# Kernel tuning notes

Hardware: AMD Instinct MI355X
Metric: run time of the kernel (lower is better)

Reference implementation:

```python
import jax, jax.numpy as jnp
import numpy as np

N_NODES = 50000
N_EDGES = 600000
D = 128
N_GRAPHS = 64


def setup_inputs() -> dict:
    key = jax.random.key(0)
    ks = jax.random.split(key, 16)
    x = jax.random.normal(ks[0], (N_NODES, D), dtype=jnp.float32)
    edge_index = jax.random.randint(ks[1], (2, N_EDGES), 0, N_NODES, dtype=jnp.int64)
    batch = jnp.sort(jax.random.randint(ks[2], (N_NODES,), 0, N_GRAPHS, dtype=jnp.int64))
    s = 1.0 / np.sqrt(D)
    def lin(k, out_d, in_d):
        return jax.random.uniform(k, (out_d, in_d), jnp.float32, -s, s)
    inp = {"x": x, "edge_index": edge_index, "batch": batch}
    for i, base in zip(range(3), (3, 6, 9)):
        inp[f"W_rel{i+1}"] = lin(ks[base], D, D)
        inp[f"b_rel{i+1}"] = jax.random.uniform(ks[base + 1], (D,), jnp.float32, -s, s)
        inp[f"W_root{i+1}"] = lin(ks[base + 2], D, D)
    s5 = 1.0 / np.sqrt(5)
    inp["W1"] = lin(ks[12], 5, D)
    inp["b1"] = jax.random.uniform(ks[13], (5,), jnp.float32, -s, s)
    inp["W2"] = jax.random.uniform(ks[14], (1, 5), jnp.float32, -s5, s5)
    inp["b2"] = jax.random.uniform(ks[15], (1,), jnp.float32, -s5, s5)
    return inp


def graph_conv(x, src, dst, W_rel, b_rel, W_root):
    # PyG GraphConv: out_i = W_root x_i + W_rel * sum_{j->i} x_j + b_rel
    agg = jax.ops.segment_sum(x[src], dst, num_segments=N_NODES)  # [N, D]
    return agg @ W_rel.T + b_rel + x @ W_root.T


def reference(x, edge_index, batch,
              W_rel1, b_rel1, W_root1,
              W_rel2, b_rel2, W_root2,
              W_rel3, b_rel3, W_root3,
              W1, b1, W2, b2):
    src, dst = edge_index[0], edge_index[1]
    h = jax.nn.relu(graph_conv(x, src, dst, W_rel1, b_rel1, W_root1))
    h = jax.nn.relu(graph_conv(h, src, dst, W_rel2, b_rel2, W_root2))
    h = graph_conv(h, src, dst, W_rel3, b_rel3, W_root3)
    # global max pool over graphs
    g = jax.ops.segment_max(h, batch, num_segments=N_GRAPHS)  # [G, D]
    out = jax.nn.relu(g @ W1.T + b1) @ W2.T + b2  # [G, 1]
    return out
```

## Files before the change

kernel.cpp:

```cpp
#include <hip/hip_runtime.h>
#include <float.h>

#define N_NODES 50000
#define N_EDGES 600000
#define D 128
#define N_GRAPHS 64
#define SCAN_T 256
#define SCAN_NBLK ((N_NODES + SCAN_T - 1) / SCAN_T)

typedef __attribute__((ext_vector_type(8))) short short8;
typedef __attribute__((ext_vector_type(4))) float floatx4;

__device__ inline float bf2f(unsigned short h) {
    return __uint_as_float((unsigned)h << 16);
}
__device__ inline unsigned short f2bf(float f) {
    unsigned u = __float_as_uint(f);
    return (unsigned short)((u + 0x7fffu + ((u >> 16) & 1u)) >> 16);
}

#define ACCQ(u, ss) {                                                            \
    int w0_ = (u).x, w1_ = (u).y, w2_ = (u).z, w3_ = (u).w;                      \
    a[ 0] += (float)(signed char)(w0_      ) * (ss);                             \
    a[ 1] += (float)(signed char)(w0_ >>  8) * (ss);                             \
    a[ 2] += (float)(signed char)(w0_ >> 16) * (ss);                             \
    a[ 3] += (float)(w0_ >> 24)              * (ss);                             \
    a[ 4] += (float)(signed char)(w1_      ) * (ss);                             \
    a[ 5] += (float)(signed char)(w1_ >>  8) * (ss);                             \
    a[ 6] += (float)(signed char)(w1_ >> 16) * (ss);                             \
    a[ 7] += (float)(w1_ >> 24)              * (ss);                             \
    a[ 8] += (float)(signed char)(w2_      ) * (ss);                             \
    a[ 9] += (float)(signed char)(w2_ >>  8) * (ss);                             \
    a[10] += (float)(signed char)(w2_ >> 16) * (ss);                             \
    a[11] += (float)(w2_ >> 24)              * (ss);                             \
    a[12] += (float)(signed char)(w3_      ) * (ss);                             \
    a[13] += (float)(signed char)(w3_ >>  8) * (ss);                             \
    a[14] += (float)(signed char)(w3_ >> 16) * (ss);                             \
    a[15] += (float)(w3_ >> 24)              * (ss); }


__global__ __launch_bounds__(256) void cast_prep(
    const float* __restrict__ x,
    unsigned short* __restrict__ xb, signed char* __restrict__ xq,
    float* __restrict__ xs,
    const float* __restrict__ Wr0, const float* __restrict__ Wo0,
    const float* __restrict__ Wr1, const float* __restrict__ Wo1,
    const float* __restrict__ Wr2, const float* __restrict__ Wo2,
    unsigned short* __restrict__ B0, unsigned short* __restrict__ B1,
    unsigned short* __restrict__ B2,
    int* __restrict__ deg, float* __restrict__ g)
{
    int t = blockIdx.x * 256 + threadIdx.x;
    if (t < N_NODES * 16) {
        int node = t >> 4, ln = t & 15;
        const float4* xr = (const float4*)(x + (size_t)node * D + ln * 8);
        float4 v0 = xr[0], v1 = xr[1];
        float v[8] = {v0.x, v0.y, v0.z, v0.w, v1.x, v1.y, v1.z, v1.w};
        float am = 0.f;
#pragma unroll
        for (int i = 0; i < 8; ++i) am = fmaxf(am, fabsf(v[i]));
#pragma unroll
        for (int m = 1; m < 16; m <<= 1) am = fmaxf(am, __shfl_xor(am, m, 16));
        float inv = (am > 0.f) ? 127.f / am : 0.f;
        short8 hb;
#pragma unroll
        for (int i = 0; i < 8; ++i) hb[i] = (short)f2bf(v[i]);
        *(short8*)(xb + (size_t)node * D + ln * 8) = hb;
        int q0 = 0, q1 = 0;
#pragma unroll
        for (int i = 0; i < 4; ++i) { int q = (int)rintf(v[i]     * inv); q0 |= (q & 0xff) << (8 * i); }
#pragma unroll
        for (int i = 0; i < 4; ++i) { int q = (int)rintf(v[4 + i] * inv); q1 |= (q & 0xff) << (8 * i); }
        int2 qp; qp.x = q0; qp.y = q1;
        *(int2*)(xq + (size_t)node * D + ln * 8) = qp;
        if (ln == 0) xs[node] = am * (1.f / 127.f);
        return;
    }
    int w = t - N_NODES * 16;
    if (w < 3 * 128 * 256) {
        int l = w >> 15;
        int r = w & 32767;
        int o = r >> 8, k = r & 255;
        const float* Wr = (l == 0) ? Wr0 : (l == 1) ? Wr1 : Wr2;
        const float* Wo = (l == 0) ? Wo0 : (l == 1) ? Wo1 : Wo2;
        unsigned short* B = (l == 0) ? B0 : (l == 1) ? B1 : B2;
        float v = (k < 128) ? Wr[o * 128 + k] : Wo[o * 128 + (k - 128)];
        B[r] = f2bf(v);
        return;
    }
    w -= 3 * 128 * 256;
    if (w < N_NODES) { deg[w] = 0; return; }
    w -= N_NODES;
    if (w < N_GRAPHS * D) g[w] = -FLT_MAX;
}


__global__ void count_deg(const int* __restrict__ ei, int* __restrict__ deg) {
    int e = blockIdx.x * 256 + threadIdx.x;
    if (e < N_EDGES) atomicAdd(&deg[ei[N_EDGES + e]], 1);
}

__global__ __launch_bounds__(SCAN_T) void block_sum(const int* __restrict__ deg,
                                                    int* __restrict__ blockSums) {
    __shared__ int s[SCAN_T];
    int tid = threadIdx.x;
    int i = blockIdx.x * SCAN_T + tid;
    s[tid] = (i < N_NODES) ? deg[i] : 0;
    __syncthreads();
    for (int off = SCAN_T / 2; off > 0; off >>= 1) {
        if (tid < off) s[tid] += s[tid + off];
        __syncthreads();
    }
    if (tid == 0) blockSums[blockIdx.x] = s[0];
}

__global__ __launch_bounds__(SCAN_T) void scan_write(const int* __restrict__ deg,
                                                     const int* __restrict__ blockSums,
                                                     int* __restrict__ row_start,
                                                     int* __restrict__ cursor) {
    __shared__ int bs[SCAN_T];
    __shared__ int s[SCAN_T];
    int tid = threadIdx.x;
    bs[tid] = (tid < SCAN_NBLK) ? blockSums[tid] : 0;
    __syncthreads();
    for (int off = 1; off < SCAN_T; off <<= 1) {
        int tt = (tid >= off) ? bs[tid - off] : 0;
        __syncthreads();
        bs[tid] += tt;
        __syncthreads();
    }
    int myOff = (blockIdx.x == 0) ? 0 : bs[blockIdx.x - 1];
    if (blockIdx.x == 0 && tid == SCAN_T - 1) row_start[N_NODES] = bs[tid];

    int i = blockIdx.x * SCAN_T + tid;
    int v = (i < N_NODES) ? deg[i] : 0;
    s[tid] = v;
    __syncthreads();
    for (int off = 1; off < SCAN_T; off <<= 1) {
        int tt = (tid >= off) ? s[tid - off] : 0;
        __syncthreads();
        s[tid] += tt;
        __syncthreads();
    }
    if (i < N_NODES) {
        int rs = myOff + s[tid] - v;
        row_start[i] = rs;
        cursor[i]    = rs;
    }
}

__global__ void fill_csr(const int* __restrict__ ei, int* __restrict__ cursor,
                         int* __restrict__ csr_src) {
    int e = blockIdx.x * 256 + threadIdx.x;
    if (e < N_EDGES) {
        int dst = ei[N_EDGES + e];
        int pos = atomicAdd(&cursor[dst], 1);
        csr_src[pos] = ei[e];
    }
}


__global__ __launch_bounds__(256) void gather_q(
    const signed char* __restrict__ xq, const float* __restrict__ xs,
    const int* __restrict__ row_start, const int* __restrict__ csr_src,
    unsigned short* __restrict__ aggb)
{
    int grp  = threadIdx.x >> 3;
    int ln   = threadIdx.x & 7;
    int node = blockIdx.x * 32 + grp;
    if (node >= N_NODES) return;
    int beg = row_start[node];
    int end = row_start[node + 1];

    float a[16];
#pragma unroll
    for (int i = 0; i < 16; ++i) a[i] = 0.f;

    for (int base = beg; base < end; base += 8) {
        int n = end - base; if (n > 8) n = 8;
        int idx = (ln < n) ? csr_src[base + ln] : 0;
        int j = 0;
        for (; j + 3 < n; j += 4) {
            int s0 = __shfl(idx, j,     8); int s1 = __shfl(idx, j + 1, 8);
            int s2 = __shfl(idx, j + 2, 8); int s3 = __shfl(idx, j + 3, 8);
            int4 u0 = *(const int4*)(xq + (size_t)s0 * D + ln * 16);
            int4 u1 = *(const int4*)(xq + (size_t)s1 * D + ln * 16);
            int4 u2 = *(const int4*)(xq + (size_t)s2 * D + ln * 16);
            int4 u3 = *(const int4*)(xq + (size_t)s3 * D + ln * 16);
            float ss0 = xs[s0], ss1 = xs[s1], ss2 = xs[s2], ss3 = xs[s3];
            ACCQ(u0, ss0); ACCQ(u1, ss1); ACCQ(u2, ss2); ACCQ(u3, ss3);
        }
        for (; j < n; ++j) {
            int s0 = __shfl(idx, j, 8);
            int4 u0 = *(const int4*)(xq + (size_t)s0 * D + ln * 16);
            float ss0 = xs[s0];
            ACCQ(u0, ss0);
        }
    }
    short8 r0, r1;
#pragma unroll
    for (int i = 0; i < 8; ++i) { r0[i] = (short)f2bf(a[i]); r1[i] = (short)f2bf(a[8 + i]); }
    *(short8*)(aggb + (size_t)node * D + ln * 16)     = r0;
    *(short8*)(aggb + (size_t)node * D + ln * 16 + 8) = r1;
}


__device__ inline void stage_b_half(unsigned short* sB, const unsigned short* __restrict__ Bb,
                                    int tid, int h) {
#pragma unroll
    for (int i = 0; i < 8; ++i) {
        int flat = tid + i * 256;
        int fi = flat >> 6, ln = flat & 63;
        int mm = ln & 15, qq = ln >> 4;
        int ksL = fi >> 3, tt = fi & 7;
        short8 v = *(const short8*)(Bb + (size_t)(tt * 16 + mm) * 256
                                    + (h * 4 + ksL) * 32 + qq * 8);
        *(short8*)(sB + (size_t)flat * 8) = v;
    }
}


struct GemmShared {
    union {
        unsigned short b[16384];
        float c[64 * 130];
    };
};

__global__ __launch_bounds__(256) void gemm_mfma(
    const unsigned short* __restrict__ aggb, const unsigned short* __restrict__ xb,
    const unsigned short* __restrict__ Bb, const float* __restrict__ bias,
    unsigned short* __restrict__ Ob, signed char* __restrict__ Oq,
    float* __restrict__ Os)
{
    __shared__ GemmShared sh;
    int tid  = threadIdx.x;
    int wave = tid >> 6;
    int lane = tid & 63;
    int m    = lane & 15;
    int quad = lane >> 4;
    int row0 = blockIdx.x * 64 + wave * 16;

    int arow = row0 + m;
    if (arow > N_NODES - 1) arow = N_NODES - 1;

    short8 af[8];
#pragma unroll
    for (int ks = 0; ks < 8; ++ks) {
        const unsigned short* Asrc = (ks < 4) ? aggb : xb;
        af[ks] = *(const short8*)(Asrc + (size_t)arow * 128 + (ks & 3) * 32 + quad * 8);
    }

    floatx4 acc[8];
#pragma unroll
    for (int t = 0; t < 8; ++t) acc[t] = (floatx4){0.f, 0.f, 0.f, 0.f};

    stage_b_half(sh.b, Bb, tid, 0);
    __syncthreads();
#pragma unroll
    for (int ksL = 0; ksL < 4; ++ksL)
#pragma unroll
        for (int t = 0; t < 8; ++t) {
            short8 b = *(const short8*)(sh.b + (size_t)((ksL * 8 + t) * 64 + lane) * 8);
            acc[t] = __builtin_amdgcn_mfma_f32_16x16x32_bf16(af[ksL], b, acc[t], 0, 0, 0);
        }
    __syncthreads();
    stage_b_half(sh.b, Bb, tid, 1);
    __syncthreads();
#pragma unroll
    for (int ksL = 0; ksL < 4; ++ksL)
#pragma unroll
        for (int t = 0; t < 8; ++t) {
            short8 b = *(const short8*)(sh.b + (size_t)((ksL * 8 + t) * 64 + lane) * 8);
            acc[t] = __builtin_amdgcn_mfma_f32_16x16x32_bf16(af[4 + ksL], b, acc[t], 0, 0, 0);
        }
    __syncthreads();

#pragma unroll
    for (int t = 0; t < 8; ++t) {
        int col = t * 16 + m;
        float bv = bias[col];
#pragma unroll
        for (int r = 0; r < 4; ++r) {
            float v = fmaxf(acc[t][r] + bv, 0.f);
            sh.c[(wave * 16 + quad * 4 + r) * 130 + col] = v;
        }
    }
    __syncthreads();

    int lr  = tid >> 2;
    int seg = tid & 3;
    int grow = blockIdx.x * 64 + lr;
    const float* cp = &sh.c[lr * 130 + seg * 32];
    float vv[32];
    float am = 0.f;
#pragma unroll
    for (int i = 0; i < 32; ++i) { vv[i] = cp[i]; am = fmaxf(am, fabsf(vv[i])); }
    am = fmaxf(am, __shfl_xor(am, 1));
    am = fmaxf(am, __shfl_xor(am, 2));
    float inv = (am > 0.f) ? 127.f / am : 0.f;

    if (grow < N_NODES) {
#pragma unroll
        for (int c8 = 0; c8 < 4; ++c8) {
            short8 hb;
#pragma unroll
            for (int i = 0; i < 8; ++i) hb[i] = (short)f2bf(vv[c8 * 8 + i]);
            *(short8*)(Ob + (size_t)grow * 128 + seg * 32 + c8 * 8) = hb;
        }
        int qd[8];
#pragma unroll
        for (int d = 0; d < 8; ++d) {
            int q = 0;
#pragma unroll
            for (int i = 0; i < 4; ++i) {
                int qq = (int)rintf(vv[d * 4 + i] * inv);
                q |= (qq & 0xff) << (8 * i);
            }
            qd[d] = q;
        }
        int4 p0; p0.x = qd[0]; p0.y = qd[1]; p0.z = qd[2]; p0.w = qd[3];
        int4 p1; p1.x = qd[4]; p1.y = qd[5]; p1.z = qd[6]; p1.w = qd[7];
        *(int4*)(Oq + (size_t)grow * 128 + seg * 32)      = p0;
        *(int4*)(Oq + (size_t)grow * 128 + seg * 32 + 16) = p1;
        if (seg == 0) Os[grow] = am * (1.f / 127.f);
    }
}


struct PoolShared {
    union {
        unsigned short b[16384];
        float c[64 * 129];
    };
};

__global__ __launch_bounds__(256) void gemm_pool(
    const unsigned short* __restrict__ aggb, const unsigned short* __restrict__ xb,
    const unsigned short* __restrict__ Bb, const float* __restrict__ bias,
    const int* __restrict__ batch, float* __restrict__ g)
{
    __shared__ PoolShared sh;
    __shared__ int bl[64];
    int tid  = threadIdx.x;
    int wave = tid >> 6;
    int lane = tid & 63;
    int m    = lane & 15;
    int quad = lane >> 4;
    int row0 = blockIdx.x * 64;

    int arow = row0 + wave * 16 + m;
    if (arow > N_NODES - 1) arow = N_NODES - 1;

    short8 af[8];
#pragma unroll
    for (int ks = 0; ks < 8; ++ks) {
        const unsigned short* Asrc = (ks < 4) ? aggb : xb;
        af[ks] = *(const short8*)(Asrc + (size_t)arow * 128 + (ks & 3) * 32 + quad * 8);
    }

    floatx4 acc[8];
#pragma unroll
    for (int t = 0; t < 8; ++t) acc[t] = (floatx4){0.f, 0.f, 0.f, 0.f};

    if (tid < 64) {
        int grow = row0 + tid;
        bl[tid] = (grow < N_NODES) ? batch[grow] : -1;
    }
    stage_b_half(sh.b, Bb, tid, 0);
    __syncthreads();
#pragma unroll
    for (int ksL = 0; ksL < 4; ++ksL)
#pragma unroll
        for (int t = 0; t < 8; ++t) {
            short8 b = *(const short8*)(sh.b + (size_t)((ksL * 8 + t) * 64 + lane) * 8);
            acc[t] = __builtin_amdgcn_mfma_f32_16x16x32_bf16(af[ksL], b, acc[t], 0, 0, 0);
        }
    __syncthreads();
    stage_b_half(sh.b, Bb, tid, 1);
    __syncthreads();
#pragma unroll
    for (int ksL = 0; ksL < 4; ++ksL)
#pragma unroll
        for (int t = 0; t < 8; ++t) {
            short8 b = *(const short8*)(sh.b + (size_t)((ksL * 8 + t) * 64 + lane) * 8);
            acc[t] = __builtin_amdgcn_mfma_f32_16x16x32_bf16(af[4 + ksL], b, acc[t], 0, 0, 0);
        }
    __syncthreads();

#pragma unroll
    for (int t = 0; t < 8; ++t) {
        int col = t * 16 + m;
        float bv = bias[col];
#pragma unroll
        for (int r = 0; r < 4; ++r)
            sh.c[(wave * 16 + quad * 4 + r) * 129 + col] = acc[t][r] + bv;
    }
    __syncthreads();

    int nvalid = min(64, N_NODES - row0);
    int b0 = bl[0], b1 = bl[nvalid - 1];
    int col  = tid & 127;
    int rbeg = (tid >> 7) * 32;
    for (int gg = b0; gg <= b1; ++gg) {
        float cur = -FLT_MAX;
#pragma unroll
        for (int r = 0; r < 32; ++r) {
            int rr = rbeg + r;
            float v = (bl[rr] == gg) ? sh.c[rr * 129 + col] : -FLT_MAX;
            cur = fmaxf(cur, v);
        }
        if (cur > -FLT_MAX) {
            float* ad = &g[gg * D + col];
            if (cur >= 0.f) atomicMax((int*)ad, __float_as_int(cur));
            else            atomicMin((unsigned int*)ad, __float_as_uint(cur));
        }
    }
}


__global__ __launch_bounds__(64) void mlp_head(const float* __restrict__ g,
                         const float* __restrict__ W1, const float* __restrict__ b1,
                         const float* __restrict__ W2, const float* __restrict__ b2,
                         float* __restrict__ out) {
    int gi = blockIdx.x;
    int lane = threadIdx.x;
    float x0 = g[gi * D + lane];
    float x1 = g[gi * D + 64 + lane];
    float o = b2[0];
#pragma unroll
    for (int j = 0; j < 5; ++j) {
        float p = x0 * W1[j * D + lane] + x1 * W1[j * D + 64 + lane];
#pragma unroll
        for (int off = 32; off > 0; off >>= 1) p += __shfl_xor(p, off, 64);
        o += fmaxf(p + b1[j], 0.f) * W2[j];
    }
    if (lane == 0) out[gi] = o;
}

extern "C" void kernel_launch(void* const* d_in, const int* in_sizes, int n_in,
                              void* d_out, int out_size, void* d_ws, size_t ws_size,
                              hipStream_t stream) {
    const float* x     = (const float*)d_in[0];
    const int*   ei    = (const int*)d_in[1];
    const int*   batch = (const int*)d_in[2];
    const float* Wrel[3]  = {(const float*)d_in[3], (const float*)d_in[6], (const float*)d_in[9]};
    const float* brel[3]  = {(const float*)d_in[4], (const float*)d_in[7], (const float*)d_in[10]};
    const float* Wroot[3] = {(const float*)d_in[5], (const float*)d_in[8], (const float*)d_in[11]};
    const float* W1 = (const float*)d_in[12];
    const float* b1 = (const float*)d_in[13];
    const float* W2 = (const float*)d_in[14];
    const float* b2 = (const float*)d_in[15];
    float* out = (float*)d_out;

    char* ws = (char*)d_ws;
    const size_t nodeB16 = (size_t)N_NODES * D * sizeof(unsigned short);
    const size_t nodeB8  = (size_t)N_NODES * D;
    unsigned short* xb   = (unsigned short*)(ws);
    unsigned short* h1b  = (unsigned short*)(ws + 1 * nodeB16);
    unsigned short* h2b  = (unsigned short*)(ws + 2 * nodeB16);
    unsigned short* aggb = (unsigned short*)(ws + 3 * nodeB16);
    char* p = ws + 4 * nodeB16;
    signed char* xq  = (signed char*)p;  p += nodeB8;
    signed char* h1q = (signed char*)p;  p += nodeB8;
    signed char* h2q = (signed char*)p;  p += nodeB8;
    float* xs  = (float*)p;  p += N_NODES * sizeof(float);
    float* h1s = (float*)p;  p += N_NODES * sizeof(float);
    float* h2s = (float*)p;  p += N_NODES * sizeof(float);
    unsigned short* Bb0 = (unsigned short*)p;   p += 128 * 256 * sizeof(unsigned short);
    unsigned short* Bb1 = (unsigned short*)p;   p += 128 * 256 * sizeof(unsigned short);
    unsigned short* Bb2 = (unsigned short*)p;   p += 128 * 256 * sizeof(unsigned short);
    float* g        = (float*)p;                p += N_GRAPHS * D * sizeof(float);
    int*   deg      = (int*)p;                  p += N_NODES * sizeof(int);
    int*   row_start= (int*)p;                  p += (N_NODES + 1) * sizeof(int);
    int*   cursor   = (int*)p;                  p += N_NODES * sizeof(int);
    int*   csr_src  = (int*)p;                  p += N_EDGES * sizeof(int);
    int*   blockSums= (int*)p;                  p += SCAN_NBLK * sizeof(int);

    const int cast_total = N_NODES * 16 + 3 * 128 * 256 + N_NODES + N_GRAPHS * D;
    cast_prep<<<(cast_total + 255) / 256, 256, 0, stream>>>(
        x, xb, xq, xs,
        Wrel[0], Wroot[0], Wrel[1], Wroot[1], Wrel[2], Wroot[2],
        Bb0, Bb1, Bb2, deg, g);

    count_deg<<<(N_EDGES + 255) / 256, 256, 0, stream>>>(ei, deg);
    block_sum<<<SCAN_NBLK, SCAN_T, 0, stream>>>(deg, blockSums);
    scan_write<<<SCAN_NBLK, SCAN_T, 0, stream>>>(deg, blockSums, row_start, cursor);
    fill_csr<<<(N_EDGES + 255) / 256, 256, 0, stream>>>(ei, cursor, csr_src);

    const int ggrid = (N_NODES + 31) / 32;
    const int mgrid = (N_NODES + 63) / 64;

    gather_q<<<ggrid, 256, 0, stream>>>(xq, xs, row_start, csr_src, aggb);
    gemm_mfma<<<mgrid, 256, 0, stream>>>(aggb, xb, Bb0, brel[0], h1b, h1q, h1s);
    gather_q<<<ggrid, 256, 0, stream>>>(h1q, h1s, row_start, csr_src, aggb);
    gemm_mfma<<<mgrid, 256, 0, stream>>>(aggb, h1b, Bb1, brel[1], h2b, h2q, h2s);
    gather_q<<<ggrid, 256, 0, stream>>>(h2q, h2s, row_start, csr_src, aggb);
    gemm_pool<<<mgrid, 256, 0, stream>>>(aggb, h2b, Bb2, brel[2], batch, g);

    mlp_head<<<N_GRAPHS, 64, 0, stream>>>(g, W1, b1, W2, b2, out);
}
```

Before: 320.4 us.

## Fuse neighbor gather into MFMA layer kernels and drop bf16 feature copies

The separate gather kernel is folded into each layer's GEMM kernel. Each lane now accumulates its MFMA A-fragment directly from int8 neighbor rows, which removes the bf16 aggregate buffer round trip and three launches. The root term is also taken from the int8 features, dequantized in registers, so bf16 copies of x/h1/h2 are no longer written. In exchange, the root term now uses int8-quantized features, which costs accuracy. The gather also gets a less coalesced access pattern: 4 separate 8-byte loads per row per lane, while degree imbalance now serializes within the 16 rows of a wave.

```diff
diff --git a/kernel.cpp b/kernel.cpp
--- a/kernel.cpp
+++ b/kernel.cpp
@@ -19,30 +19,35 @@
     return (unsigned short)((u + 0x7fffu + ((u >> 16) & 1u)) >> 16);
 }
 
-#define ACCQ(u, ss) {                                                            \
-    int w0_ = (u).x, w1_ = (u).y, w2_ = (u).z, w3_ = (u).w;                      \
-    a[ 0] += (float)(signed char)(w0_      ) * (ss);                             \
-    a[ 1] += (float)(signed char)(w0_ >>  8) * (ss);                             \
-    a[ 2] += (float)(signed char)(w0_ >> 16) * (ss);                             \
-    a[ 3] += (float)(w0_ >> 24)              * (ss);                             \
-    a[ 4] += (float)(signed char)(w1_      ) * (ss);                             \
-    a[ 5] += (float)(signed char)(w1_ >>  8) * (ss);                             \
-    a[ 6] += (float)(signed char)(w1_ >> 16) * (ss);                             \
-    a[ 7] += (float)(w1_ >> 24)              * (ss);                             \
-    a[ 8] += (float)(signed char)(w2_      ) * (ss);                             \
-    a[ 9] += (float)(signed char)(w2_ >>  8) * (ss);                             \
-    a[10] += (float)(signed char)(w2_ >> 16) * (ss);                             \
-    a[11] += (float)(w2_ >> 24)              * (ss);                             \
-    a[12] += (float)(signed char)(w3_      ) * (ss);                             \
-    a[13] += (float)(signed char)(w3_ >>  8) * (ss);                             \
-    a[14] += (float)(signed char)(w3_ >> 16) * (ss);                             \
-    a[15] += (float)(w3_ >> 24)              * (ss); }
+
+__device__ inline void acc8v(int2 u, float ss, float* a) {
+    a[0] += (float)(signed char)(u.x      ) * ss;
+    a[1] += (float)(signed char)(u.x >>  8) * ss;
+    a[2] += (float)(signed char)(u.x >> 16) * ss;
+    a[3] += (float)(u.x >> 24)              * ss;
+    a[4] += (float)(signed char)(u.y      ) * ss;
+    a[5] += (float)(signed char)(u.y >>  8) * ss;
+    a[6] += (float)(signed char)(u.y >> 16) * ss;
+    a[7] += (float)(u.y >> 24)              * ss;
+}
+
+__device__ inline short8 deq8(int2 u, float ss) {
+    short8 r;
+    r[0] = (short)f2bf((float)(signed char)(u.x      ) * ss);
+    r[1] = (short)f2bf((float)(signed char)(u.x >>  8) * ss);
+    r[2] = (short)f2bf((float)(signed char)(u.x >> 16) * ss);
+    r[3] = (short)f2bf((float)(u.x >> 24)              * ss);
+    r[4] = (short)f2bf((float)(signed char)(u.y      ) * ss);
+    r[5] = (short)f2bf((float)(signed char)(u.y >>  8) * ss);
+    r[6] = (short)f2bf((float)(signed char)(u.y >> 16) * ss);
+    r[7] = (short)f2bf((float)(u.y >> 24)              * ss);
+    return r;
+}
 
 
 __global__ __launch_bounds__(256) void cast_prep(
     const float* __restrict__ x,
-    unsigned short* __restrict__ xb, signed char* __restrict__ xq,
-    float* __restrict__ xs,
+    signed char* __restrict__ xq, float* __restrict__ xs,
     const float* __restrict__ Wr0, const float* __restrict__ Wo0,
     const float* __restrict__ Wr1, const float* __restrict__ Wo1,
     const float* __restrict__ Wr2, const float* __restrict__ Wo2,
@@ -62,10 +67,6 @@
 #pragma unroll
         for (int m = 1; m < 16; m <<= 1) am = fmaxf(am, __shfl_xor(am, m, 16));
         float inv = (am > 0.f) ? 127.f / am : 0.f;
-        short8 hb;
-#pragma unroll
-        for (int i = 0; i < 8; ++i) hb[i] = (short)f2bf(v[i]);
-        *(short8*)(xb + (size_t)node * D + ln * 8) = hb;
         int q0 = 0, q1 = 0;
 #pragma unroll
         for (int i = 0; i < 4; ++i) { int q = (int)rintf(v[i]     * inv); q0 |= (q & 0xff) << (8 * i); }
@@ -160,48 +161,32 @@
 }
 
 
-__global__ __launch_bounds__(256) void gather_q(
-    const signed char* __restrict__ xq, const float* __restrict__ xs,
-    const int* __restrict__ row_start, const int* __restrict__ csr_src,
-    unsigned short* __restrict__ aggb)
+__device__ inline void gather_frag(const signed char* __restrict__ xq,
+                                   const float* __restrict__ xs,
+                                   const int* __restrict__ row_start,
+                                   const int* __restrict__ csr_src,
+                                   int node, int m, int quad, float* a)
 {
-    int grp  = threadIdx.x >> 3;
-    int ln   = threadIdx.x & 7;
-    int node = blockIdx.x * 32 + grp;
+#pragma unroll
+    for (int i = 0; i < 32; ++i) a[i] = 0.f;
     if (node >= N_NODES) return;
     int beg = row_start[node];
     int end = row_start[node + 1];
-
-    float a[16];
-#pragma unroll
-    for (int i = 0; i < 16; ++i) a[i] = 0.f;
-
-    for (int base = beg; base < end; base += 8) {
-        int n = end - base; if (n > 8) n = 8;
-        int idx = (ln < n) ? csr_src[base + ln] : 0;
-        int j = 0;
-        for (; j + 3 < n; j += 4) {
-            int s0 = __shfl(idx, j,     8); int s1 = __shfl(idx, j + 1, 8);
-            int s2 = __shfl(idx, j + 2, 8); int s3 = __shfl(idx, j + 3, 8);
-            int4 u0 = *(const int4*)(xq + (size_t)s0 * D + ln * 16);
-            int4 u1 = *(const int4*)(xq + (size_t)s1 * D + ln * 16);
-            int4 u2 = *(const int4*)(xq + (size_t)s2 * D + ln * 16);
-            int4 u3 = *(const int4*)(xq + (size_t)s3 * D + ln * 16);
-            float ss0 = xs[s0], ss1 = xs[s1], ss2 = xs[s2], ss3 = xs[s3];
-            ACCQ(u0, ss0); ACCQ(u1, ss1); ACCQ(u2, ss2); ACCQ(u3, ss3);
-        }
-        for (; j < n; ++j) {
-            int s0 = __shfl(idx, j, 8);
-            int4 u0 = *(const int4*)(xq + (size_t)s0 * D + ln * 16);
-            float ss0 = xs[s0];
-            ACCQ(u0, ss0);
-        }
-    }
-    short8 r0, r1;
-#pragma unroll
-    for (int i = 0; i < 8; ++i) { r0[i] = (short)f2bf(a[i]); r1[i] = (short)f2bf(a[8 + i]); }
-    *(short8*)(aggb + (size_t)node * D + ln * 16)     = r0;
-    *(short8*)(aggb + (size_t)node * D + ln * 16 + 8) = r1;
+    for (int base = beg; base < end; base += 4) {
+        int n = end - base; if (n > 4) n = 4;
+        int idx = (quad < n) ? csr_src[base + quad] : 0;
+        for (int j = 0; j < n; ++j) {
+            int s = __shfl(idx, m + 16 * j, 64);
+            const signed char* rp = xq + (size_t)s * D + quad * 8;
+            int2 q0 = *(const int2*)(rp);
+            int2 q1 = *(const int2*)(rp + 32);
+            int2 q2 = *(const int2*)(rp + 64);
+            int2 q3 = *(const int2*)(rp + 96);
+            float ss = xs[s];
+            acc8v(q0, ss, a); acc8v(q1, ss, a + 8);
+            acc8v(q2, ss, a + 16); acc8v(q3, ss, a + 24);
+        }
+    }
 }
 
 
@@ -227,11 +212,11 @@
     };
 };
 
-__global__ __launch_bounds__(256) void gemm_mfma(
-    const unsigned short* __restrict__ aggb, const unsigned short* __restrict__ xb,
+__global__ __launch_bounds__(256) void layer_fused(
+    const signed char* __restrict__ xq, const float* __restrict__ xs,
+    const int* __restrict__ row_start, const int* __restrict__ csr_src,
     const unsigned short* __restrict__ Bb, const float* __restrict__ bias,
-    unsigned short* __restrict__ Ob, signed char* __restrict__ Oq,
-    float* __restrict__ Os)
+    signed char* __restrict__ Oq, float* __restrict__ Os)
 {
     __shared__ GemmShared sh;
     int tid  = threadIdx.x;
@@ -240,16 +225,28 @@
     int m    = lane & 15;
     int quad = lane >> 4;
     int row0 = blockIdx.x * 64 + wave * 16;
-
-    int arow = row0 + m;
-    if (arow > N_NODES - 1) arow = N_NODES - 1;
-
-    short8 af[8];
-#pragma unroll
-    for (int ks = 0; ks < 8; ++ks) {
-        const unsigned short* Asrc = (ks < 4) ? aggb : xb;
-        af[ks] = *(const short8*)(Asrc + (size_t)arow * 128 + (ks & 3) * 32 + quad * 8);
-    }
+    int node = row0 + m;
+
+    float a[32];
+    gather_frag(xq, xs, row_start, csr_src, node, m, quad, a);
+
+    short8 afA[4];
+#pragma unroll
+    for (int ks = 0; ks < 4; ++ks) {
+        short8 f;
+#pragma unroll
+        for (int j = 0; j < 8; ++j) f[j] = (short)f2bf(a[ks * 8 + j]);
+        afA[ks] = f;
+    }
+
+    int arow = (node < N_NODES) ? node : N_NODES - 1;
+    const signed char* xr = xq + (size_t)arow * D + quad * 8;
+    float fsr = xs[arow];
+    short8 afX[4];
+    afX[0] = deq8(*(const int2*)(xr),      fsr);
+    afX[1] = deq8(*(const int2*)(xr + 32), fsr);
+    afX[2] = deq8(*(const int2*)(xr + 64), fsr);
+    afX[3] = deq8(*(const int2*)(xr + 96), fsr);
 
     floatx4 acc[8];
 #pragma unroll
@@ -262,7 +259,7 @@
 #pragma unroll
         for (int t = 0; t < 8; ++t) {
             short8 b = *(const short8*)(sh.b + (size_t)((ksL * 8 + t) * 64 + lane) * 8);
-            acc[t] = __builtin_amdgcn_mfma_f32_16x16x32_bf16(af[ksL], b, acc[t], 0, 0, 0);
+            acc[t] = __builtin_amdgcn_mfma_f32_16x16x32_bf16(afA[ksL], b, acc[t], 0, 0, 0);
         }
     __syncthreads();
     stage_b_half(sh.b, Bb, tid, 1);
@@ -272,7 +269,7 @@
 #pragma unroll
         for (int t = 0; t < 8; ++t) {
             short8 b = *(const short8*)(sh.b + (size_t)((ksL * 8 + t) * 64 + lane) * 8);
-            acc[t] = __builtin_amdgcn_mfma_f32_16x16x32_bf16(af[4 + ksL], b, acc[t], 0, 0, 0);
+            acc[t] = __builtin_amdgcn_mfma_f32_16x16x32_bf16(afX[ksL], b, acc[t], 0, 0, 0);
         }
     __syncthreads();
 
@@ -281,10 +278,8 @@
         int col = t * 16 + m;
         float bv = bias[col];
 #pragma unroll
-        for (int r = 0; r < 4; ++r) {
-            float v = fmaxf(acc[t][r] + bv, 0.f);
-            sh.c[(wave * 16 + quad * 4 + r) * 130 + col] = v;
-        }
+        for (int r = 0; r < 4; ++r)
+            sh.c[(wave * 16 + quad * 4 + r) * 130 + col] = fmaxf(acc[t][r] + bv, 0.f);
     }
     __syncthreads();
 
@@ -301,13 +296,6 @@
     float inv = (am > 0.f) ? 127.f / am : 0.f;
 
     if (grow < N_NODES) {
-#pragma unroll
-        for (int c8 = 0; c8 < 4; ++c8) {
-            short8 hb;
-#pragma unroll
-            for (int i = 0; i < 8; ++i) hb[i] = (short)f2bf(vv[c8 * 8 + i]);
-            *(short8*)(Ob + (size_t)grow * 128 + seg * 32 + c8 * 8) = hb;
-        }
         int qd[8];
 #pragma unroll
         for (int d = 0; d < 8; ++d) {
@@ -335,8 +323,9 @@
     };
 };
 
-__global__ __launch_bounds__(256) void gemm_pool(
-    const unsigned short* __restrict__ aggb, const unsigned short* __restrict__ xb,
+__global__ __launch_bounds__(256) void layer_pool(
+    const signed char* __restrict__ xq, const float* __restrict__ xs,
+    const int* __restrict__ row_start, const int* __restrict__ csr_src,
     const unsigned short* __restrict__ Bb, const float* __restrict__ bias,
     const int* __restrict__ batch, float* __restrict__ g)
 {
@@ -348,16 +337,28 @@
     int m    = lane & 15;
     int quad = lane >> 4;
     int row0 = blockIdx.x * 64;
-
-    int arow = row0 + wave * 16 + m;
-    if (arow > N_NODES - 1) arow = N_NODES - 1;
-
-    short8 af[8];
-#pragma unroll
-    for (int ks = 0; ks < 8; ++ks) {
-        const unsigned short* Asrc = (ks < 4) ? aggb : xb;
-        af[ks] = *(const short8*)(Asrc + (size_t)arow * 128 + (ks & 3) * 32 + quad * 8);
-    }
+    int node = row0 + wave * 16 + m;
+
+    float a[32];
+    gather_frag(xq, xs, row_start, csr_src, node, m, quad, a);
+
+    short8 afA[4];
+#pragma unroll
+    for (int ks = 0; ks < 4; ++ks) {
+        short8 f;
+#pragma unroll
+        for (int j = 0; j < 8; ++j) f[j] = (short)f2bf(a[ks * 8 + j]);
+        afA[ks] = f;
+    }
+
+    int arow = (node < N_NODES) ? node : N_NODES - 1;
+    const signed char* xr = xq + (size_t)arow * D + quad * 8;
+    float fsr = xs[arow];
+    short8 afX[4];
+    afX[0] = deq8(*(const int2*)(xr),      fsr);
+    afX[1] = deq8(*(const int2*)(xr + 32), fsr);
+    afX[2] = deq8(*(const int2*)(xr + 64), fsr);
+    afX[3] = deq8(*(const int2*)(xr + 96), fsr);
 
     floatx4 acc[8];
 #pragma unroll
@@ -374,7 +375,7 @@
 #pragma unroll
         for (int t = 0; t < 8; ++t) {
             short8 b = *(const short8*)(sh.b + (size_t)((ksL * 8 + t) * 64 + lane) * 8);
-            acc[t] = __builtin_amdgcn_mfma_f32_16x16x32_bf16(af[ksL], b, acc[t], 0, 0, 0);
+            acc[t] = __builtin_amdgcn_mfma_f32_16x16x32_bf16(afA[ksL], b, acc[t], 0, 0, 0);
         }
     __syncthreads();
     stage_b_half(sh.b, Bb, tid, 1);
@@ -384,7 +385,7 @@
 #pragma unroll
         for (int t = 0; t < 8; ++t) {
             short8 b = *(const short8*)(sh.b + (size_t)((ksL * 8 + t) * 64 + lane) * 8);
-            acc[t] = __builtin_amdgcn_mfma_f32_16x16x32_bf16(af[4 + ksL], b, acc[t], 0, 0, 0);
+            acc[t] = __builtin_amdgcn_mfma_f32_16x16x32_bf16(afX[ksL], b, acc[t], 0, 0, 0);
         }
     __syncthreads();
 
@@ -454,16 +455,11 @@
     float* out = (float*)d_out;
 
     char* ws = (char*)d_ws;
-    const size_t nodeB16 = (size_t)N_NODES * D * sizeof(unsigned short);
-    const size_t nodeB8  = (size_t)N_NODES * D;
-    unsigned short* xb   = (unsigned short*)(ws);
-    unsigned short* h1b  = (unsigned short*)(ws + 1 * nodeB16);
-    unsigned short* h2b  = (unsigned short*)(ws + 2 * nodeB16);
-    unsigned short* aggb = (unsigned short*)(ws + 3 * nodeB16);
-    char* p = ws + 4 * nodeB16;
-    signed char* xq  = (signed char*)p;  p += nodeB8;
-    signed char* h1q = (signed char*)p;  p += nodeB8;
-    signed char* h2q = (signed char*)p;  p += nodeB8;
+    const size_t nodeB8 = (size_t)N_NODES * D;
+    signed char* xq  = (signed char*)(ws);
+    signed char* h1q = (signed char*)(ws + 1 * nodeB8);
+    signed char* h2q = (signed char*)(ws + 2 * nodeB8);
+    char* p = ws + 3 * nodeB8;
     float* xs  = (float*)p;  p += N_NODES * sizeof(float);
     float* h1s = (float*)p;  p += N_NODES * sizeof(float);
     float* h2s = (float*)p;  p += N_NODES * sizeof(float);
@@ -479,7 +475,7 @@
 
     const int cast_total = N_NODES * 16 + 3 * 128 * 256 + N_NODES + N_GRAPHS * D;
     cast_prep<<<(cast_total + 255) / 256, 256, 0, stream>>>(
-        x, xb, xq, xs,
+        x, xq, xs,
         Wrel[0], Wroot[0], Wrel[1], Wroot[1], Wrel[2], Wroot[2],
         Bb0, Bb1, Bb2, deg, g);
 
@@ -488,15 +484,11 @@
     scan_write<<<SCAN_NBLK, SCAN_T, 0, stream>>>(deg, blockSums, row_start, cursor);
     fill_csr<<<(N_EDGES + 255) / 256, 256, 0, stream>>>(ei, cursor, csr_src);
 
-    const int ggrid = (N_NODES + 31) / 32;
     const int mgrid = (N_NODES + 63) / 64;
 
-    gather_q<<<ggrid, 256, 0, stream>>>(xq, xs, row_start, csr_src, aggb);
-    gemm_mfma<<<mgrid, 256, 0, stream>>>(aggb, xb, Bb0, brel[0], h1b, h1q, h1s);
-    gather_q<<<ggrid, 256, 0, stream>>>(h1q, h1s, row_start, csr_src, aggb);
-    gemm_mfma<<<mgrid, 256, 0, stream>>>(aggb, h1b, Bb1, brel[1], h2b, h2q, h2s);
-    gather_q<<<ggrid, 256, 0, stream>>>(h2q, h2s, row_start, csr_src, aggb);
-    gemm_pool<<<mgrid, 256, 0, stream>>>(aggb, h2b, Bb2, brel[2], batch, g);
+    layer_fused<<<mgrid, 256, 0, stream>>>(xq,  xs,  row_start, csr_src, Bb0, brel[0], h1q, h1s);
+    layer_fused<<<mgrid, 256, 0, stream>>>(h1q, h1s, row_start, csr_src, Bb1, brel[1], h2q, h2s);
+    layer_pool <<<mgrid, 256, 0, stream>>>(h2q, h2s, row_start, csr_src, Bb2, brel[2], batch, g);
 
     mlp_head<<<N_GRAPHS, 64, 0, stream>>>(g, W1, b1, W2, b2, out);
 }
```

After: 338.8 us. 5.7% more time.
